# Optimization experiments

Hardware: AMD Instinct MI355X
Metric: run time of the kernel (lower is better)

## Reference

```python
import jax, jax.numpy as jnp
import numpy as np

HEADS, DIM_HEAD = 8, 64  # per init_kwargs


def cdist(x, w):
    """Euclidean distance between rows of x [..., n, d] and w [m, d] -> [..., n, m].
    Matches torch.cdist (non-squared) / L2DistanceLinear(squared=False)."""
    sq = (x * x).sum(-1, keepdims=True) + (w * w).sum(-1) - 2.0 * (x @ w.T)
    return jnp.sqrt(jnp.maximum(sq, 0.0))


def setup_inputs() -> dict:
    key = jax.random.key(0)
    k1, k2, k3 = jax.random.split(key, 3)
    B, N, D = 4, 2048, 512
    dim_inner = HEADS * DIM_HEAD  # 512
    x = jax.random.normal(k1, (B, N, D), dtype=jnp.float32)
    w_qkv = jax.random.normal(k2, (3 * dim_inner, D), dtype=jnp.float32)
    w_out = jax.random.normal(k3, (D, dim_inner), dtype=jnp.float32)
    return {"x": x, "w_qkv": w_qkv, "w_out": w_out}


def reference(x, w_qkv, w_out):
    B, N, D = x.shape
    scale = DIM_HEAD ** -0.5

    # L2-distance QKV projection (cdist, non-squared, no negate/bias)
    qkv = cdist(x, w_qkv)                                  # [B, N, 3*H*DH]
    qkv = qkv.reshape(B, N, 3, HEADS, DIM_HEAD).transpose(2, 0, 3, 1, 4)  # [3, B, H, N, DH]
    q, k, v = qkv[0], qkv[1], qkv[2]

    # neg squared-L2 attention scores: -(||q||^2 + ||k||^2 - 2 q.k)
    q_sq = (q * q).sum(-1)                                 # [B, H, N]
    k_sq = (k * k).sum(-1)                                 # [B, H, N]
    dots = jnp.einsum('bhid,bhjd->bhij', q, k)             # [B, H, N, N]
    sim = -(q_sq[..., :, None] + k_sq[..., None, :] - 2.0 * dots) * scale

    attn = jax.nn.softmax(sim, axis=-1)
    out = jnp.einsum('bhij,bhjd->bhid', attn, v)           # [B, H, N, DH]
    out = out.transpose(0, 2, 1, 3).reshape(B, N, HEADS * DIM_HEAD)

    # L2-distance output projection
    return cdist(out, w_out)                               # [B, N, D]
```

## Files before the change

kernel.cpp:

```cpp
#include <hip/hip_runtime.h>
#include <stdint.h>

typedef float v4f  __attribute__((ext_vector_type(4)));
typedef float v16f __attribute__((ext_vector_type(16)));
typedef short v8s  __attribute__((ext_vector_type(8)));
typedef uint32_t u32;

#define DEVI static __device__ __forceinline__

DEVI unsigned short f2bf(float f) {
    u32 u = __builtin_bit_cast(u32, f);
    u = (u + 0x7fffu + ((u >> 16) & 1u)) >> 16;
    return (unsigned short)u;
}
DEVI float bf2f(unsigned short h) {
    u32 u = ((u32)h) << 16;
    return __builtin_bit_cast(float, u);
}

template <typename T>
DEVI void async16(const T* g, T* l) {
    __builtin_amdgcn_global_load_lds(
        (const __attribute__((address_space(1))) u32*)g,
        (__attribute__((address_space(3))) u32*)l, 16, 0, 0);
}

DEVI v4f bmfma(v8s a, v8s b, v4f c) {
    return __builtin_amdgcn_mfma_f32_16x16x32_bf16(a, b, c, 0, 0, 0);
}
DEVI v16f bmfma32(v8s a, v8s b, v16f c) {
    return __builtin_amdgcn_mfma_f32_32x32x16_bf16(a, b, c, 0, 0, 0);
}

#if __has_builtin(__builtin_amdgcn_permlane32_swap)
#define HAVE_PLSWAP 1
typedef unsigned int v2u __attribute__((ext_vector_type(2)));
#endif

DEVI void swap32(u32 a, u32 b, u32& lo, u32& hi) {
#ifdef HAVE_PLSWAP
    v2u r = __builtin_amdgcn_permlane32_swap(a, b, false, false);
    lo = r.x; hi = r.y;
#else
    u32 ax = __shfl_xor(a, 32), bx = __shfl_xor(b, 32);
    int hh = (threadIdx.x & 63) >> 5;
    lo = hh ? bx : a;
    hi = hh ? b : ax;
#endif
}

static const size_t HSZ = 32ull * 2048 * 64;

__launch_bounds__(256, 2)
__global__ void prep_rows(const float* __restrict__ X, unsigned short* __restrict__ Xb,
                          float* __restrict__ Sq, float* __restrict__ Rs, int hasRs)
{
    const int w = threadIdx.x >> 6, lane = threadIdx.x & 63;
    const int r = blockIdx.x * 4 + w;
    const float* xr = X + (size_t)r * 512 + lane * 8;
    float4 a = *(const float4*)xr;
    float4 c = *(const float4*)(xr + 4);
    float s = a.x*a.x + a.y*a.y + a.z*a.z + a.w*a.w
            + c.x*c.x + c.y*c.y + c.z*c.z + c.w*c.w;
    float sm = a.x + a.y + a.z + a.w + c.x + c.y + c.z + c.w;
    uint4 pkv;
    unsigned short* e = (unsigned short*)&pkv;
    e[0] = f2bf(a.x); e[1] = f2bf(a.y); e[2] = f2bf(a.z); e[3] = f2bf(a.w);
    e[4] = f2bf(c.x); e[5] = f2bf(c.y); e[6] = f2bf(c.z); e[7] = f2bf(c.w);
    *(uint4*)(Xb + (size_t)r * 512 + lane * 8) = pkv;
#pragma unroll
    for (int d = 32; d > 0; d >>= 1) {
        s  += __shfl_xor(s, d);
        sm += __shfl_xor(sm, d);
    }
    if (lane == 0) { Sq[r] = s; if (hasRs) Rs[r] = sm; }
}

__launch_bounds__(256, 2)
__global__ void outsq_kernel(const unsigned short* __restrict__ Op, float* __restrict__ Osq)
{
    const int w = threadIdx.x >> 6, lane = threadIdx.x & 63;
    const int r = blockIdx.x * 4 + w;
    uint4 pk = *(const uint4*)(Op + (size_t)r * 512 + lane * 8);
    const unsigned short* e = (const unsigned short*)&pk;
    float s = 0.f;
#pragma unroll
    for (int u = 0; u < 8; ++u) { float f = bf2f(e[u]) + 32.f; s += f * f; }
#pragma unroll
    for (int d = 32; d > 0; d >>= 1) s += __shfl_xor(s, d);
    if (lane == 0) Osq[r] = s;
}

__launch_bounds__(256, 2)
__global__ void gemm_cdist(const unsigned short* __restrict__ A,
                           const unsigned short* __restrict__ B,
                           const float* __restrict__ Asq,
                           const float* __restrict__ Bsq,
                           unsigned short* __restrict__ QKV,
                           float* __restrict__ Ksqc)
{
    __shared__ unsigned short lsm[2 * 128 * 64];
    unsigned short* lA = lsm;
    unsigned short* lB = lsm + 128 * 64;
    const int t = threadIdx.x;
    const int lane = t & 63, w = t >> 6;
    const int low = lane & 15, quad = lane >> 4;
    const int wm = w & 1, wn = w >> 1;
    const int tM = blockIdx.x * 128, tN = blockIdx.y * 128;

    v4f acc[4][4];
#pragma unroll
    for (int a = 0; a < 4; ++a)
#pragma unroll
        for (int b = 0; b < 4; ++b) acc[a][b] = (v4f){0.f, 0.f, 0.f, 0.f};

    for (int kt = 0; kt < 512; kt += 64) {
        __syncthreads();
#pragma unroll
        for (int is = 0; is < 4; ++is) {
            int slot = is * 256 + t;
            int r = slot >> 3, bp = slot & 7;
            int bs = bp ^ (r & 7);
            async16(A + (size_t)(tM + r) * 512 + kt + bs * 8, lA + slot * 8);
            async16(B + (size_t)(tN + r) * 512 + kt + bs * 8, lB + slot * 8);
        }
        __syncthreads();

        v8s bfr[4][2];
#pragma unroll
        for (int ns = 0; ns < 4; ++ns) {
            int row = wn * 64 + ns * 16 + low;
#pragma unroll
            for (int kc = 0; kc < 2; ++kc)
                bfr[ns][kc] = *(const v8s*)(lB + (row * 8 + ((kc * 4 + quad) ^ (row & 7))) * 8);
        }
#pragma unroll
        for (int ms = 0; ms < 4; ++ms) {
            int row = wm * 64 + ms * 16 + low;
            v8s af0 = *(const v8s*)(lA + (row * 8 + ((0 + quad) ^ (row & 7))) * 8);
            v8s af1 = *(const v8s*)(lA + (row * 8 + ((4 + quad) ^ (row & 7))) * 8);
#pragma unroll
            for (int ns = 0; ns < 4; ++ns) {
                acc[ms][ns] = bmfma(af0, bfr[ns][0], acc[ms][ns]);
                acc[ms][ns] = bmfma(af1, bfr[ns][1], acc[ms][ns]);
            }
        }
    }

    const int tt = tN >> 9;
    if (tt != 2) {
#pragma unroll
        for (int ms = 0; ms < 4; ++ms) {
#pragma unroll
            for (int reg = 0; reg < 4; ++reg) {
                const int row = tM + wm * 64 + ms * 16 + quad * 4 + reg;
                const int b = row >> 11, i = row & 2047;
                float kacc = 0.f;
#pragma unroll
                for (int ns = 0; ns < 4; ++ns) {
                    const int col = tN + wn * 64 + ns * 16 + low;
                    float dot = acc[ms][ns][reg];
                    float val = sqrtf(fmaxf(Asq[row] + Bsq[col] - 2.f * dot, 0.f)) - 32.f;
                    int h = (col >> 6) & 7, d = col & 63, bh = b * 8 + h;
                    if (tt == 0) {
                        QKV[((size_t)bh * 2048 + i) * 64 + d] =
                            f2bf(val * 0.36067376022224085f);
                    } else {
                        QKV[HSZ + ((size_t)bh * 2048 + i) * 64 + d] = f2bf(val);
                        kacc += val * val;
                    }
                }
                if (tt == 1) {
#pragma unroll
                    for (int d = 1; d < 16; d <<= 1) kacc += __shfl_xor(kacc, d);
                    if (low == 0) {
                        int h = ((tN + wn * 64) >> 6) & 7;
                        Ksqc[(size_t)(b * 8 + h) * 2048 + i] = kacc * 0.18033688011112042f;
                    }
                }
            }
        }
    } else {
        u32 packed[4][4][2];
#pragma unroll
        for (int ms = 0; ms < 4; ++ms)
#pragma unroll
            for (int ns = 0; ns < 4; ++ns) {
                const int col = tN + wn * 64 + ns * 16 + low;
                float bs_ = Bsq[col];
#pragma unroll
                for (int rp = 0; rp < 2; ++rp) {
                    u32 pk = 0;
#pragma unroll
                    for (int sub = 0; sub < 2; ++sub) {
                        int reg = rp * 2 + sub;
                        int row = tM + wm * 64 + ms * 16 + quad * 4 + reg;
                        float val = sqrtf(fmaxf(Asq[row] + bs_
                                                - 2.f * acc[ms][ns][reg], 0.f)) - 32.f;
                        pk |= (u32)f2bf(val) << (16 * sub);
                    }
                    packed[ms][ns][rp] = pk;
                }
            }
        u32* lT32 = (u32*)lsm;
#pragma unroll
        for (int p = 0; p < 2; ++p) {
            __syncthreads();
            if (wm == p) {
#pragma unroll
                for (int ms = 0; ms < 4; ++ms)
#pragma unroll
                    for (int ns = 0; ns < 4; ++ns) {
                        int cl = wn * 64 + ns * 16 + low;
#pragma unroll
                        for (int rp = 0; rp < 2; ++rp)
                            lT32[cl * 36 + ms * 8 + quad * 2 + rp] = packed[ms][ns][rp];
                    }
            }
            __syncthreads();
#pragma unroll
            for (int cc = 0; cc < 4; ++cc) {
                int col = cc * 32 + (t >> 3);
                int i0 = (t & 7) * 8;
                uint4 vvv = *(const uint4*)(lsm + col * 72 + i0);
                int colg = tN + col;
                int h = (colg >> 6) & 7, d = colg & 63;
                int rowg = tM + p * 64 + i0;
                int b = rowg >> 11, i = rowg & 2047;
                *(uint4*)(QKV + 2 * HSZ
                          + ((size_t)((b * 8 + h) * 64 + d)) * 2048 + i) = vvv;
            }
        }
    }
    (void)0;
}

__launch_bounds__(256, 2)
__global__ void flash_attn(const unsigned short* __restrict__ Q,
                           const unsigned short* __restrict__ K,
                           const unsigned short* __restrict__ VT,
                           const float* __restrict__ Ksqc,
                           unsigned short* __restrict__ PO,
                           float* __restrict__ PL)
{
    __shared__ unsigned short lK[64 * 64];
    __shared__ unsigned short lV[64 * 64];
    __shared__ float lKq[64];
    const int t = threadIdx.x, lane = t & 63, w = t >> 6;
    const int i31 = lane & 31, h = lane >> 5;
    const int qt = blockIdx.x, bh = blockIdx.y, sp = blockIdx.z;
    const size_t base = (size_t)bh * (2048 * 64);
    const int row0 = qt * 128 + w * 32;
    const int j0 = sp * 1024;

    v8s qfr[4];
#pragma unroll
    for (int kt = 0; kt < 4; ++kt)
        qfr[kt] = *(const v8s*)(Q + base + (size_t)(row0 + i31) * 64 + kt * 16 + h * 8);

    float nmq;
    {
        float s = 0.f;
#pragma unroll
        for (int kt = 0; kt < 4; ++kt) {
            const unsigned short* qe = (const unsigned short*)&qfr[kt];
#pragma unroll
            for (int u = 0; u < 8; ++u) { float f = bf2f(qe[u]); s += f * f; }
        }
        s += __shfl_xor(s, 32);
        nmq = -s * 1.3862943611198906f;
    }

    v16f o[2];
    float lacc = 0.f;
#pragma unroll
    for (int dt = 0; dt < 2; ++dt)
#pragma unroll
        for (int r = 0; r < 16; ++r) o[dt][r] = 0.f;

    const unsigned short* kg = K + base + (size_t)j0 * 64;
    const unsigned short* vg = VT + (size_t)bh * 64 * 2048 + j0;
    const float* kqg = Ksqc + (size_t)bh * 2048 + j0;

    for (int iter = 0; iter < 16; ++iter) {
        __syncthreads();
#pragma unroll
        for (int is = 0; is < 2; ++is) {
            int slot = is * 256 + t;
            int r = slot >> 3, bp = slot & 7, bs = bp ^ (r & 7);
            async16(kg + (size_t)r * 64 + bs * 8, lK + slot * 8);
        }
#pragma unroll
        for (int is = 0; is < 2; ++is) {
            int slot = is * 256 + t;
            int r = slot >> 3, bp = slot & 7, bs = bp ^ (r & 7);
            async16(vg + (size_t)r * 2048 + bs * 8, lV + slot * 8);
        }
        if (t < 16) async16(kqg + t * 4, lKq + t * 4);
        __syncthreads();
        kg += 64 * 64; vg += 64; kqg += 64;

#pragma unroll
        for (int T = 0; T < 2; ++T) {
            const int jrow = T * 32 + i31;
            v8s kf[4];
#pragma unroll
            for (int kt = 0; kt < 4; ++kt)
                kf[kt] = *(const v8s*)(lK + (jrow * 8 + ((2 * kt + h) ^ (jrow & 7))) * 8);
            v4f kqv[4];
#pragma unroll
            for (int r1 = 0; r1 < 4; ++r1)
                kqv[r1] = *(const v4f*)(lKq + T * 32 + r1 * 8 + h * 4);

            v16f sa;
#pragma unroll
            for (int r = 0; r < 16; ++r) sa[r] = nmq - kqv[r >> 2][r & 3];
#pragma unroll
            for (int kt = 0; kt < 4; ++kt)
                sa = bmfma32(kf[kt], qfr[kt], sa);
            u32 pk[8];
#pragma unroll
            for (int r1 = 0; r1 < 4; ++r1) {
                float p0 = exp2f(sa[4 * r1 + 0]);
                float p1 = exp2f(sa[4 * r1 + 1]);
                float p2 = exp2f(sa[4 * r1 + 2]);
                float p3 = exp2f(sa[4 * r1 + 3]);
                lacc += (p0 + p1) + (p2 + p3);
                pk[2 * r1] = __builtin_amdgcn_perm(
                    __builtin_bit_cast(u32, p1), __builtin_bit_cast(u32, p0),
                    0x07060302u);
                pk[2 * r1 + 1] = __builtin_amdgcn_perm(
                    __builtin_bit_cast(u32, p3), __builtin_bit_cast(u32, p2),
                    0x07060302u);
            }
#pragma unroll
            for (int c2 = 0; c2 < 2; ++c2) {
                const int jb = 2 * (2 * T + c2);
                v8s vf[2];
#pragma unroll
                for (int dt = 0; dt < 2; ++dt) {
                    const int drow = dt * 32 + i31;
                    vf[dt] = *(const v8s*)(lV + (drow * 8 + ((jb + h) ^ (drow & 7))) * 8);
                }
                uint4 dd;
                swap32(pk[4 * c2 + 0], pk[4 * c2 + 2], dd.x, dd.z);
                swap32(pk[4 * c2 + 1], pk[4 * c2 + 3], dd.y, dd.w);
                v8s af = __builtin_bit_cast(v8s, dd);
                o[0] = bmfma32(af, vf[0], o[0]);
                o[1] = bmfma32(af, vf[1], o[1]);
            }
        }
    }

    const int pb = (qt * 32 + bh) * 2 + sp;
    unsigned short* pob = PO + (size_t)pb * 8192;
    lacc += __shfl_xor(lacc, 32);
#pragma unroll
    for (int dt = 0; dt < 2; ++dt)
#pragma unroll
        for (int r = 0; r < 16; ++r) {
            int rl = w * 32 + (r & 3) + 8 * (r >> 2) + 4 * h;
            pob[rl * 64 + dt * 32 + i31] = f2bf(o[dt][r]);
        }
    if (h == 0)
        PL[(size_t)pb * 128 + w * 32 + i31] = lacc;
}

__launch_bounds__(256, 2)
__global__ void combine_kernel(const unsigned short* __restrict__ PO,
                               const float* __restrict__ PL,
                               unsigned short* __restrict__ O)
{
    const int qt = blockIdx.x, bh = blockIdx.y, t = threadIdx.x;
    const int b = bh >> 3, h = bh & 7;
    const int pbase = ((qt >> 1) * 32 + bh) * 2;
    const int rl = (qt & 1) * 64 + (t >> 2), c0 = (t & 3) * 16;
    float inv = 1.f / (PL[(size_t)pbase * 128 + rl] + PL[(size_t)(pbase + 1) * 128 + rl]);
    const unsigned short* a = PO + (size_t)pbase * 8192 + rl * 64 + c0;
    const unsigned short* bb = a + 8192;
    uint4 a0 = *(const uint4*)a,  a1 = *(const uint4*)(a + 8);
    uint4 b0 = *(const uint4*)bb, b1 = *(const uint4*)(bb + 8);
    const unsigned short* ae = (const unsigned short*)&a0;
    const unsigned short* be = (const unsigned short*)&b0;
    uint4 o0, o1;
    unsigned short* oe = (unsigned short*)&o0;
#pragma unroll
    for (int u = 0; u < 8; ++u) oe[u] = f2bf((bf2f(ae[u]) + bf2f(be[u])) * inv);
    ae = (const unsigned short*)&a1; be = (const unsigned short*)&b1;
    oe = (unsigned short*)&o1;
#pragma unroll
    for (int u = 0; u < 8; ++u) oe[u] = f2bf((bf2f(ae[u]) + bf2f(be[u])) * inv);
    unsigned short* dst = O + ((size_t)(b * 2048 + qt * 64 + (t >> 2))) * 512 + h * 64 + c0;
    *(uint4*)dst = o0;
    *(uint4*)(dst + 8) = o1;
}

__launch_bounds__(256, 2)
__global__ void gemm_out(const unsigned short* __restrict__ A,
                         const unsigned short* __restrict__ B,
                         const float* __restrict__ Asq,
                         const float* __restrict__ Bsq,
                         const float* __restrict__ Brs,
                         float* __restrict__ OUT)
{
    __shared__ unsigned short lA[128 * 64];
    __shared__ unsigned short lB[64 * 64];
    const int t = threadIdx.x;
    const int lane = t & 63, w = t >> 6;
    const int low = lane & 15, quad = lane >> 4;
    const int wm = w & 1, wn = w >> 1;
    const int tM = blockIdx.x * 128, tN = blockIdx.y * 64;

    v4f acc[4][2];
#pragma unroll
    for (int a = 0; a < 4; ++a)
#pragma unroll
        for (int b = 0; b < 2; ++b) acc[a][b] = (v4f){0.f, 0.f, 0.f, 0.f};

    for (int kt = 0; kt < 512; kt += 64) {
        __syncthreads();
#pragma unroll
        for (int is = 0; is < 4; ++is) {
            int slot = is * 256 + t;
            int r = slot >> 3, bp = slot & 7, bs = bp ^ (r & 7);
            async16(A + (size_t)(tM + r) * 512 + kt + bs * 8, lA + slot * 8);
        }
#pragma unroll
        for (int is = 0; is < 2; ++is) {
            int slot = is * 256 + t;
            int r = slot >> 3, bp = slot & 7, bs = bp ^ (r & 7);
            async16(B + (size_t)(tN + r) * 512 + kt + bs * 8, lB + slot * 8);
        }
        __syncthreads();

        v8s bfr[2][2];
#pragma unroll
        for (int ns = 0; ns < 2; ++ns) {
            int row = wn * 32 + ns * 16 + low;
#pragma unroll
            for (int kc = 0; kc < 2; ++kc)
                bfr[ns][kc] = *(const v8s*)(lB + (row * 8 + ((kc * 4 + quad) ^ (row & 7))) * 8);
        }
#pragma unroll
        for (int ms = 0; ms < 4; ++ms) {
            int row = wm * 64 + ms * 16 + low;
            v8s af0 = *(const v8s*)(lA + (row * 8 + ((0 + quad) ^ (row & 7))) * 8);
            v8s af1 = *(const v8s*)(lA + (row * 8 + ((4 + quad) ^ (row & 7))) * 8);
#pragma unroll
            for (int ns = 0; ns < 2; ++ns) {
                acc[ms][ns] = bmfma(af0, bfr[ns][0], acc[ms][ns]);
                acc[ms][ns] = bmfma(af1, bfr[ns][1], acc[ms][ns]);
            }
        }
    }

#pragma unroll
    for (int ms = 0; ms < 4; ++ms) {
#pragma unroll
        for (int ns = 0; ns < 2; ++ns) {
#pragma unroll
            for (int reg = 0; reg < 4; ++reg) {
                int row = tM + wm * 64 + ms * 16 + quad * 4 + reg;
                int col = tN + wn * 32 + ns * 16 + low;
                float val = sqrtf(fmaxf(Asq[row] + Bsq[col]
                                        - 2.f * (acc[ms][ns][reg] + 32.f * Brs[col]), 0.f));
                OUT[(size_t)row * 512 + col] = val;
            }
        }
    }
}

extern "C" void kernel_launch(void* const* d_in, const int* in_sizes, int n_in,
                              void* d_out, int out_size, void* d_ws, size_t ws_size,
                              hipStream_t stream)
{
    const float* x    = (const float*)d_in[0];
    const float* wqkv = (const float*)d_in[1];
    const float* wout = (const float*)d_in[2];
    float* out = (float*)d_out;

    char* ws = (char*)d_ws;
    size_t off = 0;
    auto alloc = [&](size_t bytes) -> void* {
        void* p = ws + off;
        off += (bytes + 255) & ~(size_t)255;
        return p;
    };
    unsigned short* xb   = (unsigned short*)alloc(8192ull * 512 * 2);
    unsigned short* wqb  = (unsigned short*)alloc(1536ull * 512 * 2);
    unsigned short* wob  = (unsigned short*)alloc(512ull * 512 * 2);
    unsigned short* qkv  = (unsigned short*)alloc(3ull * HSZ * 2);
    unsigned short* outp = (unsigned short*)alloc(8192ull * 512 * 2);
    unsigned short* po   = (unsigned short*)alloc(1024ull * 8192 * 2);
    float* pl   = (float*)alloc(1024ull * 128 * 4);
    float* xsq  = (float*)alloc(8192 * 4);
    float* wqsq = (float*)alloc(1536 * 4);
    float* wosq = (float*)alloc(512 * 4);
    float* wors = (float*)alloc(512 * 4);
    float* ksqc = (float*)alloc(65536ull * 4);
    float* osq  = (float*)alloc(8192 * 4);

    prep_rows<<<2048, 256, 0, stream>>>(x, xb, xsq, nullptr, 0);
    prep_rows<<<384, 256, 0, stream>>>(wqkv, wqb, wqsq, nullptr, 0);
    prep_rows<<<128, 256, 0, stream>>>(wout, wob, wosq, wors, 1);

    gemm_cdist<<<dim3(64, 12), 256, 0, stream>>>(xb, wqb, xsq, wqsq, qkv, ksqc);
    flash_attn<<<dim3(16, 32, 2), 256, 0, stream>>>(qkv, qkv + HSZ, qkv + 2 * HSZ,
                                                    ksqc, po, pl);
    combine_kernel<<<dim3(32, 32), 256, 0, stream>>>(po, pl, outp);
    outsq_kernel<<<2048, 256, 0, stream>>>(outp, osq);
    gemm_out<<<dim3(64, 8), 256, 0, stream>>>(outp, wob, osq, wosq, wors, out);
}
```

Measured before the change: 188.5 us.

## Merge prep launches, fuse output norms into combine, double-buffer flash attention

The three prep_rows launches become one prep_all kernel that picks its source by block index. The separate outsq pass is removed: combine_kernel writes per-head partial squared norms, and gemm_out sums them into shared memory. Flash attention now double-buffers its K, V and K-norm tiles so the next tile loads while the current one computes. It also drops the per-row query-norm term, since softmax is unchanged by a per-row shift, and stores negated key norms so scores start directly from them. These changes save launches and global passes and hide load latency, at the cost of more LDS and a possibly larger exponent range without the query-norm shift.

```diff
diff --git a/kernel.cpp b/kernel.cpp
--- a/kernel.cpp
+++ b/kernel.cpp
@@ -52,12 +52,22 @@
 static const size_t HSZ = 32ull * 2048 * 64;
 
 __launch_bounds__(256, 2)
-__global__ void prep_rows(const float* __restrict__ X, unsigned short* __restrict__ Xb,
-                          float* __restrict__ Sq, float* __restrict__ Rs, int hasRs)
+__global__ void prep_all(const float* __restrict__ X, const float* __restrict__ WQ,
+                         const float* __restrict__ WO,
+                         unsigned short* __restrict__ Xb, unsigned short* __restrict__ WQb,
+                         unsigned short* __restrict__ WOb,
+                         float* __restrict__ xsq, float* __restrict__ wqsq,
+                         float* __restrict__ wosq, float* __restrict__ wors)
 {
+    const int bid = blockIdx.x;
     const int w = threadIdx.x >> 6, lane = threadIdx.x & 63;
-    const int r = blockIdx.x * 4 + w;
-    const float* xr = X + (size_t)r * 512 + lane * 8;
+    const float* src; unsigned short* dst; float* Sq; float* Rs = nullptr;
+    int r;
+    if (bid < 2048)      { src = X;  dst = Xb;  Sq = xsq;  r = bid * 4 + w; }
+    else if (bid < 2432) { src = WQ; dst = WQb; Sq = wqsq; r = (bid - 2048) * 4 + w; }
+    else                 { src = WO; dst = WOb; Sq = wosq; Rs = wors; r = (bid - 2432) * 4 + w; }
+
+    const float* xr = src + (size_t)r * 512 + lane * 8;
     float4 a = *(const float4*)xr;
     float4 c = *(const float4*)(xr + 4);
     float s = a.x*a.x + a.y*a.y + a.z*a.z + a.w*a.w
@@ -67,28 +77,13 @@
     unsigned short* e = (unsigned short*)&pkv;
     e[0] = f2bf(a.x); e[1] = f2bf(a.y); e[2] = f2bf(a.z); e[3] = f2bf(a.w);
     e[4] = f2bf(c.x); e[5] = f2bf(c.y); e[6] = f2bf(c.z); e[7] = f2bf(c.w);
-    *(uint4*)(Xb + (size_t)r * 512 + lane * 8) = pkv;
+    *(uint4*)(dst + (size_t)r * 512 + lane * 8) = pkv;
 #pragma unroll
     for (int d = 32; d > 0; d >>= 1) {
         s  += __shfl_xor(s, d);
         sm += __shfl_xor(sm, d);
     }
-    if (lane == 0) { Sq[r] = s; if (hasRs) Rs[r] = sm; }
-}
-
-__launch_bounds__(256, 2)
-__global__ void outsq_kernel(const unsigned short* __restrict__ Op, float* __restrict__ Osq)
-{
-    const int w = threadIdx.x >> 6, lane = threadIdx.x & 63;
-    const int r = blockIdx.x * 4 + w;
-    uint4 pk = *(const uint4*)(Op + (size_t)r * 512 + lane * 8);
-    const unsigned short* e = (const unsigned short*)&pk;
-    float s = 0.f;
-#pragma unroll
-    for (int u = 0; u < 8; ++u) { float f = bf2f(e[u]) + 32.f; s += f * f; }
-#pragma unroll
-    for (int d = 32; d > 0; d >>= 1) s += __shfl_xor(s, d);
-    if (lane == 0) Osq[r] = s;
+    if (lane == 0) { Sq[r] = s; if (Rs) Rs[r] = sm; }
 }
 
 __launch_bounds__(256, 2)
@@ -175,7 +170,7 @@
                     for (int d = 1; d < 16; d <<= 1) kacc += __shfl_xor(kacc, d);
                     if (low == 0) {
                         int h = ((tN + wn * 64) >> 6) & 7;
-                        Ksqc[(size_t)(b * 8 + h) * 2048 + i] = kacc * 0.18033688011112042f;
+                        Ksqc[(size_t)(b * 8 + h) * 2048 + i] = -kacc * 0.18033688011112042f;
                     }
                 }
             }
@@ -243,9 +238,9 @@
                            unsigned short* __restrict__ PO,
                            float* __restrict__ PL)
 {
-    __shared__ unsigned short lK[64 * 64];
-    __shared__ unsigned short lV[64 * 64];
-    __shared__ float lKq[64];
+    __shared__ unsigned short lK[2][64 * 64];
+    __shared__ unsigned short lV[2][64 * 64];
+    __shared__ float lKq[2][64];
     const int t = threadIdx.x, lane = t & 63, w = t >> 6;
     const int i31 = lane & 31, h = lane >> 5;
     const int qt = blockIdx.x, bh = blockIdx.y, sp = blockIdx.z;
@@ -258,19 +253,6 @@
     for (int kt = 0; kt < 4; ++kt)
         qfr[kt] = *(const v8s*)(Q + base + (size_t)(row0 + i31) * 64 + kt * 16 + h * 8);
 
-    float nmq;
-    {
-        float s = 0.f;
-#pragma unroll
-        for (int kt = 0; kt < 4; ++kt) {
-            const unsigned short* qe = (const unsigned short*)&qfr[kt];
-#pragma unroll
-            for (int u = 0; u < 8; ++u) { float f = bf2f(qe[u]); s += f * f; }
-        }
-        s += __shfl_xor(s, 32);
-        nmq = -s * 1.3862943611198906f;
-    }
-
     v16f o[2];
     float lacc = 0.f;
 #pragma unroll
@@ -282,23 +264,30 @@
     const unsigned short* vg = VT + (size_t)bh * 64 * 2048 + j0;
     const float* kqg = Ksqc + (size_t)bh * 2048 + j0;
 
-    for (int iter = 0; iter < 16; ++iter) {
-        __syncthreads();
+    auto STAGE = [&](int buf) {
 #pragma unroll
         for (int is = 0; is < 2; ++is) {
             int slot = is * 256 + t;
             int r = slot >> 3, bp = slot & 7, bs = bp ^ (r & 7);
-            async16(kg + (size_t)r * 64 + bs * 8, lK + slot * 8);
+            async16(kg + (size_t)r * 64 + bs * 8, &lK[buf][slot * 8]);
         }
 #pragma unroll
         for (int is = 0; is < 2; ++is) {
             int slot = is * 256 + t;
             int r = slot >> 3, bp = slot & 7, bs = bp ^ (r & 7);
-            async16(vg + (size_t)r * 2048 + bs * 8, lV + slot * 8);
-        }
-        if (t < 16) async16(kqg + t * 4, lKq + t * 4);
-        __syncthreads();
+            async16(vg + (size_t)r * 2048 + bs * 8, &lV[buf][slot * 8]);
+        }
+        if (t < 16) async16(kqg + t * 4, &lKq[buf][t * 4]);
         kg += 64 * 64; vg += 64; kqg += 64;
+    };
+
+    STAGE(0);
+    __syncthreads();
+
+#pragma unroll 2
+    for (int iter = 0; iter < 16; ++iter) {
+        const int c = iter & 1;
+        if (iter < 15) STAGE(1 - c);
 
 #pragma unroll
         for (int T = 0; T < 2; ++T) {
@@ -306,18 +295,19 @@
             v8s kf[4];
 #pragma unroll
             for (int kt = 0; kt < 4; ++kt)
-                kf[kt] = *(const v8s*)(lK + (jrow * 8 + ((2 * kt + h) ^ (jrow & 7))) * 8);
-            v4f kqv[4];
-#pragma unroll
-            for (int r1 = 0; r1 < 4; ++r1)
-                kqv[r1] = *(const v4f*)(lKq + T * 32 + r1 * 8 + h * 4);
+                kf[kt] = *(const v8s*)(&lK[c][(jrow * 8 + ((2 * kt + h) ^ (jrow & 7))) * 8]);
 
             v16f sa;
 #pragma unroll
-            for (int r = 0; r < 16; ++r) sa[r] = nmq - kqv[r >> 2][r & 3];
+            for (int r1 = 0; r1 < 4; ++r1) {
+                v4f kq = *(const v4f*)(&lKq[c][T * 32 + r1 * 8 + h * 4]);
+#pragma unroll
+                for (int u = 0; u < 4; ++u) sa[4 * r1 + u] = kq[u];
+            }
 #pragma unroll
             for (int kt = 0; kt < 4; ++kt)
                 sa = bmfma32(kf[kt], qfr[kt], sa);
+
             u32 pk[8];
 #pragma unroll
             for (int r1 = 0; r1 < 4; ++r1) {
@@ -340,7 +330,7 @@
 #pragma unroll
                 for (int dt = 0; dt < 2; ++dt) {
                     const int drow = dt * 32 + i31;
-                    vf[dt] = *(const v8s*)(lV + (drow * 8 + ((jb + h) ^ (drow & 7))) * 8);
+                    vf[dt] = *(const v8s*)(&lV[c][(drow * 8 + ((jb + h) ^ (drow & 7))) * 8]);
                 }
                 uint4 dd;
                 swap32(pk[4 * c2 + 0], pk[4 * c2 + 2], dd.x, dd.z);
@@ -350,6 +340,7 @@
                 o[1] = bmfma32(af, vf[1], o[1]);
             }
         }
+        __syncthreads();
     }
 
     const int pb = (qt * 32 + bh) * 2 + sp;
@@ -369,7 +360,8 @@
 __launch_bounds__(256, 2)
 __global__ void combine_kernel(const unsigned short* __restrict__ PO,
                                const float* __restrict__ PL,
-                               unsigned short* __restrict__ O)
+                               unsigned short* __restrict__ O,
+                               float* __restrict__ Osqp)
 {
     const int qt = blockIdx.x, bh = blockIdx.y, t = threadIdx.x;
     const int b = bh >> 3, h = bh & 7;
@@ -393,24 +385,44 @@
     unsigned short* dst = O + ((size_t)(b * 2048 + qt * 64 + (t >> 2))) * 512 + h * 64 + c0;
     *(uint4*)dst = o0;
     *(uint4*)(dst + 8) = o1;
+
+    const unsigned short* q0 = (const unsigned short*)&o0;
+    const unsigned short* q1 = (const unsigned short*)&o1;
+    float s = 0.f;
+#pragma unroll
+    for (int u = 0; u < 8; ++u) { float f = bf2f(q0[u]) + 32.f; s += f * f; }
+#pragma unroll
+    for (int u = 0; u < 8; ++u) { float f = bf2f(q1[u]) + 32.f; s += f * f; }
+    s += __shfl_xor(s, 1);
+    s += __shfl_xor(s, 2);
+    if ((t & 3) == 0)
+        Osqp[(size_t)h * 8192 + b * 2048 + qt * 64 + (t >> 2)] = s;
 }
 
 __launch_bounds__(256, 2)
 __global__ void gemm_out(const unsigned short* __restrict__ A,
                          const unsigned short* __restrict__ B,
-                         const float* __restrict__ Asq,
+                         const float* __restrict__ Osqp,
                          const float* __restrict__ Bsq,
                          const float* __restrict__ Brs,
                          float* __restrict__ OUT)
 {
     __shared__ unsigned short lA[128 * 64];
     __shared__ unsigned short lB[64 * 64];
+    __shared__ float lAsq[128];
     const int t = threadIdx.x;
     const int lane = t & 63, w = t >> 6;
     const int low = lane & 15, quad = lane >> 4;
     const int wm = w & 1, wn = w >> 1;
     const int tM = blockIdx.x * 128, tN = blockIdx.y * 64;
 
+    if (t < 128) {
+        float s = 0.f;
+#pragma unroll
+        for (int hh = 0; hh < 8; ++hh) s += Osqp[(size_t)hh * 8192 + tM + t];
+        lAsq[t] = s;
+    }
+
     v4f acc[4][2];
 #pragma unroll
     for (int a = 0; a < 4; ++a)
@@ -460,9 +472,10 @@
         for (int ns = 0; ns < 2; ++ns) {
 #pragma unroll
             for (int reg = 0; reg < 4; ++reg) {
-                int row = tM + wm * 64 + ms * 16 + quad * 4 + reg;
+                int rloc = wm * 64 + ms * 16 + quad * 4 + reg;
+                int row = tM + rloc;
                 int col = tN + wn * 32 + ns * 16 + low;
-                float val = sqrtf(fmaxf(Asq[row] + Bsq[col]
+                float val = sqrtf(fmaxf(lAsq[rloc] + Bsq[col]
                                         - 2.f * (acc[ms][ns][reg] + 32.f * Brs[col]), 0.f));
                 OUT[(size_t)row * 512 + col] = val;
             }
@@ -498,16 +511,14 @@
     float* wosq = (float*)alloc(512 * 4);
     float* wors = (float*)alloc(512 * 4);
     float* ksqc = (float*)alloc(65536ull * 4);
-    float* osq  = (float*)alloc(8192 * 4);
-
-    prep_rows<<<2048, 256, 0, stream>>>(x, xb, xsq, nullptr, 0);
-    prep_rows<<<384, 256, 0, stream>>>(wqkv, wqb, wqsq, nullptr, 0);
-    prep_rows<<<128, 256, 0, stream>>>(wout, wob, wosq, wors, 1);
+    float* osqp = (float*)alloc(8ull * 8192 * 4);
+
+    prep_all<<<2560, 256, 0, stream>>>(x, wqkv, wout, xb, wqb, wob,
+                                       xsq, wqsq, wosq, wors);
 
     gemm_cdist<<<dim3(64, 12), 256, 0, stream>>>(xb, wqb, xsq, wqsq, qkv, ksqc);
     flash_attn<<<dim3(16, 32, 2), 256, 0, stream>>>(qkv, qkv + HSZ, qkv + 2 * HSZ,
                                                     ksqc, po, pl);
-    combine_kernel<<<dim3(32, 32), 256, 0, stream>>>(po, pl, outp);
-    outsq_kernel<<<2048, 256, 0, stream>>>(outp, osq);
-    gemm_out<<<dim3(64, 8), 256, 0, stream>>>(outp, wob, osq, wosq, wors, out);
-}
+    combine_kernel<<<dim3(32, 32), 256, 0, stream>>>(po, pl, outp, osqp);
+    gemm_out<<<dim3(64, 8), 256, 0, stream>>>(outp, wob, osqp, wosq, wors, out);
+}
```

Measured after the change: 173.1 us. -8.2%, faster.
